# Kernel optimization log

Measured on AMD Instinct MI355X. Metric: run time of the kernel, lower is better.

## Reference

```python
import jax, jax.numpy as jnp
import numpy as np

B, S, D, H = 1, 2048, 768, 12
E, K, I = 8, 2, 1024          # routed experts, top-k, expert inter dim
IS = 2 * I                    # shared-expert inter dim (n_shared_experts * moe_inter_dim)
EPS = 1e-5
ROUTE_SCALE = 1.0


def rmsnorm(x, w, eps=EPS):
    xf = x.astype(jnp.float32)
    return (xf * jax.lax.rsqrt(jnp.mean(xf * xf, axis=-1, keepdims=True) + eps)).astype(x.dtype) * w


def setup_inputs() -> dict:
    key = jax.random.key(0)
    ks = jax.random.split(key, 8)
    sc = 0.02
    return {
        "x": jax.random.normal(ks[0], (B, S, D), jnp.float32),
        "norm1_w": jnp.ones((D,), jnp.float32),
        "norm3_w": jnp.ones((D,), jnp.float32),
        "gate_w": jax.random.normal(ks[1], (E, D), jnp.float32) * sc,
        "w1": jax.random.normal(ks[2], (E, I, D), jnp.float32) * sc,
        "b1": jnp.zeros((E, I), jnp.float32),
        "w2": jax.random.normal(ks[3], (E, D, I), jnp.float32) * sc,
        "b2": jnp.zeros((E, D), jnp.float32),
        "w3": jax.random.normal(ks[4], (E, I, D), jnp.float32) * sc,
        "b3": jnp.zeros((E, I), jnp.float32),
        "fc1_w": jax.random.normal(ks[5], (IS, D), jnp.float32) * sc,
        "fc1_b": jnp.zeros((IS,), jnp.float32),
        "fc2_w": jax.random.normal(ks[6], (D, IS), jnp.float32) * sc,
        "fc2_b": jnp.zeros((D,), jnp.float32),
    }


def _forward(x, norm1_w, norm3_w, gate_w, w1, b1, w2, b2, w3, b3,
             fc1_w, fc1_b, fc2_w, fc2_b):
    b, s, d = x.shape
    hd = d // H

    # ---- self-attention (no qkv/out projections in the original module) ----
    xn = rmsnorm(x, norm1_w)
    qkv = xn.reshape(b, s, H, hd).transpose(0, 2, 1, 3)      # [b,h,s,hd]
    scores = jnp.einsum("bhqd,bhkd->bhqk", qkv, qkv) / np.sqrt(hd)
    attn = jax.nn.softmax(scores, axis=-1)
    ao = jnp.einsum("bhqk,bhkd->bhqd", attn, qkv)
    attn_out = ao.transpose(0, 2, 1, 3).reshape(b, s, d)
    out = x + attn_out

    # ---- MoE on norm3(out) ----
    xf = rmsnorm(out, norm3_w).reshape(-1, d)                # [N, D]
    n = xf.shape[0]

    # Gate: softmax scoring, n_groups=1 (no group masking), no bias (dim != 7168)
    logits = xf @ gate_w.T                                    # [N, E]
    sc = jax.nn.softmax(logits.astype(jnp.float32), axis=-1)  # max-subtract folded in
    _, idx = jax.lax.top_k(sc, K)                             # [N, K]
    weights = jnp.take_along_axis(sc, idx, axis=-1)
    weights = jnp.clip(weights, 1e-7) * ROUTE_SCALE
    weights = weights.astype(xf.dtype)

    # combine matrix: per-token dense expert weights (zeros for unselected)
    cmb = jnp.zeros((n, E), xf.dtype).at[jnp.arange(n)[:, None], idx].add(weights)

    # SwiGLU experts, batched over E (zero combine weight == not dispatched)
    a = jnp.einsum("nd,eid->nei", xf, w1) + b1                # [N,E,I]
    g = jnp.einsum("nd,eid->nei", xf, w3) + b3
    h = jax.nn.silu(a) * g
    eo = jnp.einsum("nei,edi->ned", h, w2) + b2               # [N,E,D]
    y = jnp.einsum("ned,ne->nd", eo, cmb)

    # shared experts (SiLU MLP)
    z = jax.nn.silu(xf @ fc1_w.T + fc1_b) @ fc2_w.T + fc2_b

    moe_out = (y + z).reshape(b, s, d)
    return out + moe_out


def reference(x, norm1_w, norm3_w, gate_w, w1, b1, w2, b2, w3, b3,
              fc1_w, fc1_b, fc2_w, fc2_b):
    return _forward(x, norm1_w, norm3_w, gate_w, w1, b1, w2, b2, w3, b3,
                    fc1_w, fc1_b, fc2_w, fc2_b)
```

## Files before the change

kernel.cpp:

```cpp
#include <hip/hip_runtime.h>
#include <math.h>

#define SEQ    2048
#define DMODEL 768
#define NHEAD  12
#define NEXP   8
#define IDIM   1024
#define ISH    2048
#define KVS    4
#define NE2    10

typedef unsigned short u16;
typedef short s16x8 __attribute__((ext_vector_type(8)));
typedef u16   u16x8 __attribute__((ext_vector_type(8)));
typedef float f32x4 __attribute__((ext_vector_type(4)));

#define MFMA_BF16(a, b, c) __builtin_amdgcn_mfma_f32_16x16x32_bf16((a), (b), (c), 0, 0, 0)

__device__ __forceinline__ void glds16(const void* g, void* l) {
  __builtin_amdgcn_global_load_lds(
      (const __attribute__((address_space(1))) unsigned int*)g,
      (__attribute__((address_space(3))) unsigned int*)l, 16, 0, 0);
}

__device__ __forceinline__ u16 f2b(float f) {
  unsigned int u = __float_as_uint(f);
  unsigned int r = u + 0x7fffu + ((u >> 16) & 1u);
  return (u16)(r >> 16);
}
__device__ __forceinline__ float b2f(u16 v) {
  return __uint_as_float(((unsigned int)v) << 16);
}

__global__ __launch_bounds__(256) void cvt_all_kernel(
    const float* __restrict__ w1, const float* __restrict__ w3, const float* __restrict__ w2,
    const float* __restrict__ fc1, const float* __restrict__ fc2,
    u16* __restrict__ w1b, u16* __restrict__ w3b, u16* __restrict__ w2b,
    u16* __restrict__ fc1b, u16* __restrict__ fc2b, int* __restrict__ counts) {
  if (blockIdx.x == 0 && threadIdx.x < 16) counts[threadIdx.x] = 0;
  long i = (long)blockIdx.x * 256 + threadIdx.x;
  const long NW8 = (long)NEXP * IDIM * DMODEL / 8;
  const long NF8 = (long)ISH * DMODEL / 8;
  const float* s; u16* d; long o;
  if      (i < NW8)             { s = w1;  d = w1b;  o = i; }
  else if (i < 2 * NW8)         { s = w3;  d = w3b;  o = i - NW8; }
  else if (i < 3 * NW8)         { s = w2;  d = w2b;  o = i - 2 * NW8; }
  else if (i < 3 * NW8 + NF8)   { s = fc1; d = fc1b; o = i - 3 * NW8; }
  else if (i < 3 * NW8 + 2*NF8) { s = fc2; d = fc2b; o = i - 3 * NW8 - NF8; }
  else return;
  float4 a = ((const float4*)s)[2 * o], b = ((const float4*)s)[2 * o + 1];
  u16x8 v;
  v[0] = f2b(a.x); v[1] = f2b(a.y); v[2] = f2b(a.z); v[3] = f2b(a.w);
  v[4] = f2b(b.x); v[5] = f2b(b.y); v[6] = f2b(b.z); v[7] = f2b(b.w);
  ((u16x8*)d)[o] = v;
}

__global__ __launch_bounds__(256) void rmsnorm_kernel(const float* __restrict__ in,
                                                      const float* __restrict__ w,
                                                      u16* __restrict__ outb) {
  int row = blockIdx.x;
  int tid = threadIdx.x;
  const float* r = in + (size_t)row * DMODEL;
  float v0 = r[tid], v1 = r[tid + 256], v2 = r[tid + 512];
  float ss = v0 * v0 + v1 * v1 + v2 * v2;
  __shared__ float red[256];
  red[tid] = ss;
  __syncthreads();
  for (int s = 128; s > 0; s >>= 1) {
    if (tid < s) red[tid] += red[tid + s];
    __syncthreads();
  }
  float rms = rsqrtf(red[0] * (1.f / DMODEL) + 1e-5f);
  u16* ob = outb + (size_t)row * DMODEL;
  ob[tid]       = f2b(v0 * rms * w[tid]);
  ob[tid + 256] = f2b(v1 * rms * w[tid + 256]);
  ob[tid + 512] = f2b(v2 * rms * w[tid + 512]);
}

__global__ __launch_bounds__(256) void attn_kernel(const u16* __restrict__ xnb,
                                                   u16* __restrict__ Opart,
                                                   float* __restrict__ Mpart,
                                                   float* __restrict__ Lpart) {
  __shared__ u16 Qs[64][72];
  __shared__ u16 Ks[64][72];
  __shared__ u16 Vt[64][72];
  __shared__ u16 Ps[64][72];
  const int h = blockIdx.y, kvs = blockIdx.z;
  const int q0 = blockIdx.x * 64;
  const int tid = threadIdx.x;
  const int lane = tid & 63, w = tid >> 6;
  const int quad = lane >> 4, l15 = lane & 15;
  const size_t hoff = (size_t)h * 64;

  for (int cc = tid; cc < 512; cc += 256) {
    int row = cc >> 3, col8 = (cc & 7) * 8;
    *(u16x8*)&Qs[row][col8] = *(const u16x8*)(xnb + (size_t)(q0 + row) * DMODEL + hoff + col8);
  }
  __syncthreads();
  const s16x8 aq0 = *(const s16x8*)&Qs[16 * w + l15][quad * 8];
  const s16x8 aq1 = *(const s16x8*)&Qs[16 * w + l15][32 + quad * 8];

  f32x4 o[4] = {};
  float mrow[4], lrow[4];
#pragma unroll
  for (int r = 0; r < 4; r++) { mrow[r] = -INFINITY; lrow[r] = 0.f; }

  const int it0 = kvs * (SEQ / 64 / KVS);
  for (int it = 0; it < SEQ / 64 / KVS; it++) {
    const int k0 = (it0 + it) * 64;
    for (int cc = tid; cc < 512; cc += 256) {
      int row = cc >> 3, col8 = (cc & 7) * 8;
      *(u16x8*)&Ks[row][col8] = *(const u16x8*)(xnb + (size_t)(k0 + row) * DMODEL + hoff + col8);
    }
    __syncthreads();

    {
      const int rp = tid & 31, dc = ((tid >> 5) & 7) * 8;
      u16x8 v0 = *(const u16x8*)&Ks[2 * rp][dc];
      u16x8 v1 = *(const u16x8*)&Ks[2 * rp + 1][dc];
#pragma unroll
      for (int j = 0; j < 8; j++) {
        *(unsigned int*)&Vt[dc + j][2 * rp] =
            (unsigned int)v0[j] | ((unsigned int)v1[j] << 16);
      }
    }

    f32x4 s4[4] = {};
#pragma unroll
    for (int jt = 0; jt < 4; jt++) {
      s16x8 b0 = *(const s16x8*)&Ks[16 * jt + l15][quad * 8];
      s16x8 b1 = *(const s16x8*)&Ks[16 * jt + l15][32 + quad * 8];
      s4[jt] = MFMA_BF16(aq0, b0, s4[jt]);
      s4[jt] = MFMA_BF16(aq1, b1, s4[jt]);
      s4[jt] *= 0.125f;
    }

#pragma unroll
    for (int r = 0; r < 4; r++) {
      float mx = mrow[r];
#pragma unroll
      for (int jt = 0; jt < 4; jt++) mx = fmaxf(mx, s4[jt][r]);
#pragma unroll
      for (int m = 1; m <= 8; m <<= 1) mx = fmaxf(mx, __shfl_xor(mx, m, 64));
      float al = __expf(mrow[r] - mx);
      mrow[r] = mx;
      float pv[4], sum = 0.f;
#pragma unroll
      for (int jt = 0; jt < 4; jt++) { pv[jt] = __expf(s4[jt][r] - mx); sum += pv[jt]; }
#pragma unroll
      for (int m = 1; m <= 8; m <<= 1) sum += __shfl_xor(sum, m, 64);
      lrow[r] = lrow[r] * al + sum;
#pragma unroll
      for (int jt = 0; jt < 4; jt++) o[jt][r] *= al;
#pragma unroll
      for (int jt = 0; jt < 4; jt++) Ps[16 * w + quad * 4 + r][16 * jt + l15] = f2b(pv[jt]);
    }
    __syncthreads();

    s16x8 ap0 = *(const s16x8*)&Ps[16 * w + l15][quad * 8];
    s16x8 ap1 = *(const s16x8*)&Ps[16 * w + l15][32 + quad * 8];
#pragma unroll
    for (int jt = 0; jt < 4; jt++) {
      s16x8 bv0 = *(const s16x8*)&Vt[16 * jt + l15][quad * 8];
      s16x8 bv1 = *(const s16x8*)&Vt[16 * jt + l15][32 + quad * 8];
      o[jt] = MFMA_BF16(ap0, bv0, o[jt]);
      o[jt] = MFMA_BF16(ap1, bv1, o[jt]);
    }
  }

  const size_t base = ((size_t)kvs * NHEAD + h) * SEQ;
#pragma unroll
  for (int r = 0; r < 4; r++) {
    int q = q0 + 16 * w + quad * 4 + r;
#pragma unroll
    for (int jt = 0; jt < 4; jt++)
      Opart[(base + q) * 64 + 16 * jt + l15] = f2b(o[jt][r]);
    if (l15 == 0) {
      Mpart[base + q] = mrow[r];
      Lpart[base + q] = lrow[r];
    }
  }
}

__global__ __launch_bounds__(256) void fused_post_kernel(
    const u16* __restrict__ Opart, const float* __restrict__ Mpart,
    const float* __restrict__ Lpart, const float* __restrict__ x,
    const float* __restrict__ n3w, const float* __restrict__ gw,
    u16* __restrict__ xfb, float* __restrict__ out,
    int* __restrict__ counts, int* __restrict__ toklist, float* __restrict__ wtlist) {
  const int t = blockIdx.x;
  const int tid = threadIdx.x;
  __shared__ float Ms[KVS * NHEAD], Ls[KVS * NHEAD];
  __shared__ float red[256];
  __shared__ float gred[4][NEXP];
  if (tid < KVS * NHEAD) {
    Ms[tid] = Mpart[(size_t)tid * SEQ + t];
    Ls[tid] = Lpart[(size_t)tid * SEQ + t];
  }
  __syncthreads();

  float val[3];
  float ss = 0.f;
#pragma unroll
  for (int ii = 0; ii < 3; ii++) {
    int c = tid + ii * 256;
    int h = c >> 6, d = c & 63;
    float M = -INFINITY;
#pragma unroll
    for (int k = 0; k < KVS; k++) M = fmaxf(M, Ms[k * NHEAD + h]);
    float L = 0.f, O = 0.f;
#pragma unroll
    for (int k = 0; k < KVS; k++) {
      float wgt = __expf(Ms[k * NHEAD + h] - M);
      L += wgt * Ls[k * NHEAD + h];
      O += wgt * b2f(Opart[((size_t)(k * NHEAD + h) * SEQ + t) * 64 + d]);
    }
    float v = x[(size_t)t * DMODEL + c] + O / L;
    out[(size_t)t * DMODEL + c] = v;
    val[ii] = v;
    ss += v * v;
  }
  red[tid] = ss;
  __syncthreads();
  for (int s = 128; s > 0; s >>= 1) {
    if (tid < s) red[tid] += red[tid + s];
    __syncthreads();
  }
  float rms = rsqrtf(red[0] * (1.f / DMODEL) + 1e-5f);

  float ge[NEXP] = {};
#pragma unroll
  for (int ii = 0; ii < 3; ii++) {
    int c = tid + ii * 256;
    float xn = val[ii] * rms * n3w[c];
    xfb[(size_t)t * DMODEL + c] = f2b(xn);
#pragma unroll
    for (int e = 0; e < NEXP; e++) ge[e] = fmaf(xn, gw[e * DMODEL + c], ge[e]);
  }
  const int lane = tid & 63, w = tid >> 6;
#pragma unroll
  for (int off = 32; off >= 1; off >>= 1)
#pragma unroll
    for (int e = 0; e < NEXP; e++) ge[e] += __shfl_xor(ge[e], off, 64);
  if (lane == 0)
#pragma unroll
    for (int e = 0; e < NEXP; e++) gred[w][e] = ge[e];
  __syncthreads();
  if (tid == 0) {
    float p[NEXP], mx = -INFINITY, s = 0.f;
#pragma unroll
    for (int e = 0; e < NEXP; e++) {
      p[e] = gred[0][e] + gred[1][e] + gred[2][e] + gred[3][e];
      mx = fmaxf(mx, p[e]);
    }
#pragma unroll
    for (int e = 0; e < NEXP; e++) { p[e] = __expf(p[e] - mx); s += p[e]; }
    int e0 = 0; float b0 = p[0];
    for (int e = 1; e < NEXP; e++) if (p[e] > b0) { b0 = p[e]; e0 = e; }
    int e1 = -1; float b1v = -1.f;
    for (int e = 0; e < NEXP; e++) if (e != e0 && p[e] > b1v) { b1v = p[e]; e1 = e; }
    float inv = 1.f / s;
    int pos0 = atomicAdd(&counts[e0], 1);
    toklist[e0 * SEQ + pos0] = t;
    wtlist[e0 * SEQ + pos0] = fmaxf(b0 * inv, 1e-7f);
    int pos1 = atomicAdd(&counts[e1], 1);
    toklist[e1 * SEQ + pos1] = t;
    wtlist[e1 * SEQ + pos1] = fmaxf(b1v * inv, 1e-7f);
  }
}

__global__ __launch_bounds__(256) void gemm1_kernel(
    const u16* __restrict__ xfb,
    const u16* __restrict__ w1b, const u16* __restrict__ w3b, const u16* __restrict__ fc1b,
    const float* __restrict__ b1, const float* __restrict__ b3, const float* __restrict__ fc1_b,
    const int* __restrict__ counts, const int* __restrict__ toklist, u16* __restrict__ hb) {
  __shared__ u16 As[64][32];
  __shared__ u16 W1s[128][32];
  __shared__ u16 W3s[128][32];
  __shared__ int rIdx[64];
  const int e = blockIdx.z;
  const bool routed = (e < NEXP);
  int cnt, off;
  if (routed) {
    cnt = counts[e];
    off = 0;
    for (int i = 0; i < e; i++) off += counts[i];
  } else {
    cnt = SEQ;
    off = 2 * SEQ + (e - NEXP) * SEQ;
  }
  const int m0 = blockIdx.y * 64;
  if (m0 >= cnt) return;
  const int n0 = blockIdx.x * 128;
  const int tid = threadIdx.x;
  if (tid < 64) {
    int rr = m0 + tid;
    rIdx[tid] = routed ? toklist[e * SEQ + (rr < cnt ? rr : cnt - 1)] : rr;
  }
  __syncthreads();
  const u16* W1 = routed ? w1b + (size_t)e * IDIM * DMODEL
                         : fc1b + (size_t)(e - NEXP) * IDIM * DMODEL;
  const u16* W3 = w3b + (size_t)(routed ? e : 0) * IDIM * DMODEL;

  const int lane = tid & 63, w = tid >> 6;
  const int quad = lane >> 4, l15 = lane & 15;
  const int wy = w >> 1, wx = w & 1;
  const int rsub = lane >> 2, c8 = (lane & 3) * 8;
  const u16* Ap   = xfb + (size_t)rIdx[16 * w + rsub] * DMODEL + c8;
  const u16* W1p0 = W1 + (size_t)(n0 + 32 * w + rsub) * DMODEL + c8;
  const u16* W1p1 = W1 + (size_t)(n0 + 32 * w + 16 + rsub) * DMODEL + c8;
  const u16* W3p0 = W3 + (size_t)(n0 + 32 * w + rsub) * DMODEL + c8;
  const u16* W3p1 = W3 + (size_t)(n0 + 32 * w + 16 + rsub) * DMODEL + c8;

  f32x4 acc1[2][4] = {};
  f32x4 acc3[2][4] = {};
  for (int k0 = 0; k0 < DMODEL; k0 += 32) {
    glds16(Ap + k0, &As[16 * w][0]);
    glds16(W1p0 + k0, &W1s[32 * w][0]);
    glds16(W1p1 + k0, &W1s[32 * w + 16][0]);
    if (routed) {
      glds16(W3p0 + k0, &W3s[32 * w][0]);
      glds16(W3p1 + k0, &W3s[32 * w + 16][0]);
    }
    __syncthreads();
    s16x8 af[2], w1f[4];
#pragma unroll
    for (int i = 0; i < 2; i++) af[i] = *(const s16x8*)&As[32 * wy + 16 * i + l15][quad * 8];
#pragma unroll
    for (int j = 0; j < 4; j++) w1f[j] = *(const s16x8*)&W1s[64 * wx + 16 * j + l15][quad * 8];
#pragma unroll
    for (int i = 0; i < 2; i++)
#pragma unroll
      for (int j = 0; j < 4; j++)
        acc1[i][j] = MFMA_BF16(af[i], w1f[j], acc1[i][j]);
    if (routed) {
      s16x8 w3f[4];
#pragma unroll
      for (int j = 0; j < 4; j++) w3f[j] = *(const s16x8*)&W3s[64 * wx + 16 * j + l15][quad * 8];
#pragma unroll
      for (int i = 0; i < 2; i++)
#pragma unroll
        for (int j = 0; j < 4; j++)
          acc3[i][j] = MFMA_BF16(af[i], w3f[j], acc3[i][j]);
    }
    __syncthreads();
  }

#pragma unroll
  for (int j = 0; j < 4; j++) {
    int n = n0 + 64 * wx + 16 * j + l15;
    float b1v = routed ? b1[e * IDIM + n] : fc1_b[(e - NEXP) * IDIM + n];
    float b3v = routed ? b3[e * IDIM + n] : 0.f;
#pragma unroll
    for (int i = 0; i < 2; i++) {
#pragma unroll
      for (int r = 0; r < 4; r++) {
        int rr = m0 + 32 * wy + 16 * i + quad * 4 + r;
        if (rr < cnt) {
          float a = acc1[i][j][r] + b1v;
          float g = routed ? (acc3[i][j][r] + b3v) : 1.f;
          float hv = a / (1.f + __expf(-a)) * g;
          hb[(size_t)(off + rr) * IDIM + n] = f2b(hv);
        }
      }
    }
  }
}

__global__ __launch_bounds__(256) void gemm2_kernel(
    const u16* __restrict__ hb,
    const u16* __restrict__ w2b, const u16* __restrict__ fc2b,
    const float* __restrict__ b2, const float* __restrict__ fc2_b,
    const int* __restrict__ counts, const int* __restrict__ toklist,
    const float* __restrict__ wtlist, float* __restrict__ out) {
  __shared__ u16 As[64][32];
  __shared__ u16 Ws[128][32];
  const int e = blockIdx.z;
  const bool routed = (e < NEXP);
  int cnt, off;
  if (routed) {
    cnt = counts[e];
    off = 0;
    for (int i = 0; i < e; i++) off += counts[i];
  } else {
    cnt = SEQ;
    off = 2 * SEQ + (e - NEXP) * SEQ;
  }
  const int m0 = blockIdx.y * 64;
  if (m0 >= cnt) return;
  const int n0 = blockIdx.x * 128;
  const int tid = threadIdx.x;

  const u16* Wb; int ldw, kof;
  if (routed) { Wb = w2b + (size_t)e * DMODEL * IDIM; ldw = IDIM; kof = 0; }
  else        { Wb = fc2b;                            ldw = ISH;  kof = (e - NEXP) * IDIM; }

  const int lane = tid & 63, w = tid >> 6;
  const int quad = lane >> 4, l15 = lane & 15;
  const int wy = w >> 1, wx = w & 1;
  const int rsub = lane >> 2, c8 = (lane & 3) * 8;
  int ra = m0 + 16 * w + rsub; ra = off + (ra < cnt ? ra : cnt - 1);
  const u16* Ap  = hb + (size_t)ra * IDIM + c8;
  const u16* Wp0 = Wb + (size_t)(n0 + 32 * w + rsub) * ldw + kof + c8;
  const u16* Wp1 = Wb + (size_t)(n0 + 32 * w + 16 + rsub) * ldw + kof + c8;

  f32x4 acc[2][4] = {};
  for (int k0 = 0; k0 < IDIM; k0 += 32) {
    glds16(Ap + k0, &As[16 * w][0]);
    glds16(Wp0 + k0, &Ws[32 * w][0]);
    glds16(Wp1 + k0, &Ws[32 * w + 16][0]);
    __syncthreads();
    s16x8 af[2], wf[4];
#pragma unroll
    for (int i = 0; i < 2; i++) af[i] = *(const s16x8*)&As[32 * wy + 16 * i + l15][quad * 8];
#pragma unroll
    for (int j = 0; j < 4; j++) wf[j] = *(const s16x8*)&Ws[64 * wx + 16 * j + l15][quad * 8];
#pragma unroll
    for (int i = 0; i < 2; i++)
#pragma unroll
      for (int j = 0; j < 4; j++)
        acc[i][j] = MFMA_BF16(af[i], wf[j], acc[i][j]);
    __syncthreads();
  }

#pragma unroll
  for (int j = 0; j < 4; j++) {
    int n = n0 + 64 * wx + 16 * j + l15;
    float bv = routed ? b2[e * DMODEL + n] : (e == NEXP ? fc2_b[n] : 0.f);
#pragma unroll
    for (int i = 0; i < 2; i++) {
#pragma unroll
      for (int r = 0; r < 4; r++) {
        int rr = m0 + 32 * wy + 16 * i + quad * 4 + r;
        if (rr < cnt) {
          int tok; float wt;
          if (routed) { tok = toklist[e * SEQ + rr]; wt = wtlist[e * SEQ + rr]; }
          else        { tok = rr;                    wt = 1.f; }
          atomicAdd(&out[(size_t)tok * DMODEL + n], wt * (acc[i][j][r] + bv));
        }
      }
    }
  }
}

extern "C" void kernel_launch(void* const* d_in, const int* in_sizes, int n_in,
                              void* d_out, int out_size, void* d_ws, size_t ws_size,
                              hipStream_t stream) {
  const float* x       = (const float*)d_in[0];
  const float* norm1_w = (const float*)d_in[1];
  const float* norm3_w = (const float*)d_in[2];
  const float* gate_w  = (const float*)d_in[3];
  const float* w1      = (const float*)d_in[4];
  const float* b1      = (const float*)d_in[5];
  const float* w2      = (const float*)d_in[6];
  const float* b2      = (const float*)d_in[7];
  const float* w3      = (const float*)d_in[8];
  const float* b3      = (const float*)d_in[9];
  const float* fc1_w   = (const float*)d_in[10];
  const float* fc1_b   = (const float*)d_in[11];
  const float* fc2_w   = (const float*)d_in[12];
  const float* fc2_b   = (const float*)d_in[13];
  float* out = (float*)d_out;

  char* p = (char*)d_ws;
  u16*   xnb    = (u16*)p;   p += (size_t)SEQ * DMODEL * 2;
  u16*   xfb    = (u16*)p;   p += (size_t)SEQ * DMODEL * 2;
  u16*   hb     = (u16*)p;   p += (size_t)4 * SEQ * IDIM * 2;
  u16*   Opart  = (u16*)p;   p += (size_t)KVS * NHEAD * SEQ * 64 * 2;
  float* Mpart  = (float*)p; p += (size_t)KVS * NHEAD * SEQ * 4;
  float* Lpart  = (float*)p; p += (size_t)KVS * NHEAD * SEQ * 4;
  u16*   w1b    = (u16*)p;   p += (size_t)NEXP * IDIM * DMODEL * 2;
  u16*   w3b    = (u16*)p;   p += (size_t)NEXP * IDIM * DMODEL * 2;
  u16*   w2b    = (u16*)p;   p += (size_t)NEXP * DMODEL * IDIM * 2;
  u16*   fc1b   = (u16*)p;   p += (size_t)ISH * DMODEL * 2;
  u16*   fc2b   = (u16*)p;   p += (size_t)DMODEL * ISH * 2;
  int*   counts = (int*)p;   p += 256;
  int*   toklist= (int*)p;   p += (size_t)NEXP * SEQ * 4;
  float* wtlist = (float*)p; p += (size_t)NEXP * SEQ * 4;

  const long NW8 = (long)NEXP * IDIM * DMODEL / 8;
  const long NF8 = (long)ISH * DMODEL / 8;
  const int cvt_blocks = (int)((3 * NW8 + 2 * NF8 + 255) / 256);
  cvt_all_kernel<<<cvt_blocks, 256, 0, stream>>>(w1, w3, w2, fc1_w, fc2_w,
                                                 w1b, w3b, w2b, fc1b, fc2b, counts);
  rmsnorm_kernel<<<SEQ, 256, 0, stream>>>(x, norm1_w, xnb);
  attn_kernel<<<dim3(SEQ / 64, NHEAD, KVS), 256, 0, stream>>>(xnb, Opart, Mpart, Lpart);
  fused_post_kernel<<<SEQ, 256, 0, stream>>>(Opart, Mpart, Lpart, x, norm3_w, gate_w,
                                             xfb, out, counts, toklist, wtlist);
  gemm1_kernel<<<dim3(IDIM / 128, SEQ / 64, NE2), 256, 0, stream>>>(
      xfb, w1b, w3b, fc1b, b1, b3, fc1_b, counts, toklist, hb);
  gemm2_kernel<<<dim3(DMODEL / 128, SEQ / 64, NE2), 256, 0, stream>>>(
      hb, w2b, fc2b, b2, fc2_b, counts, toklist, wtlist, out);
  (void)in_sizes; (void)n_in; (void)out_size; (void)ws_size;
}
```

Baseline: 352.8 us.

## Merge weight conversion with rmsnorm, widen GEMM K-step, remap blocks per XCD

Folds the bf16 weight conversion and the first rmsnorm into one launch to save a kernel launch. Both MoE GEMMs now stage 64-wide K chunks per barrier instead of 32, halving the number of syncs and doubling MFMAs between them. The 3D grids are flattened into a 1D grid whose block index is remapped so that consecutive tiles of the same expert land on the same XCD (groups of 8), aiming at better L2 reuse of expert weights. The cost is more shared memory and registers per block, which may reduce occupancy.

```diff
diff --git a/kernel.cpp b/kernel.cpp
--- a/kernel.cpp
+++ b/kernel.cpp
@@ -32,38 +32,38 @@
   return __uint_as_float(((unsigned int)v) << 16);
 }
 
-__global__ __launch_bounds__(256) void cvt_all_kernel(
+#define CVT_BLOCKS 10752
+
+__global__ __launch_bounds__(256) void prep_kernel(
     const float* __restrict__ w1, const float* __restrict__ w3, const float* __restrict__ w2,
     const float* __restrict__ fc1, const float* __restrict__ fc2,
     u16* __restrict__ w1b, u16* __restrict__ w3b, u16* __restrict__ w2b,
-    u16* __restrict__ fc1b, u16* __restrict__ fc2b, int* __restrict__ counts) {
-  if (blockIdx.x == 0 && threadIdx.x < 16) counts[threadIdx.x] = 0;
-  long i = (long)blockIdx.x * 256 + threadIdx.x;
-  const long NW8 = (long)NEXP * IDIM * DMODEL / 8;
-  const long NF8 = (long)ISH * DMODEL / 8;
-  const float* s; u16* d; long o;
-  if      (i < NW8)             { s = w1;  d = w1b;  o = i; }
-  else if (i < 2 * NW8)         { s = w3;  d = w3b;  o = i - NW8; }
-  else if (i < 3 * NW8)         { s = w2;  d = w2b;  o = i - 2 * NW8; }
-  else if (i < 3 * NW8 + NF8)   { s = fc1; d = fc1b; o = i - 3 * NW8; }
-  else if (i < 3 * NW8 + 2*NF8) { s = fc2; d = fc2b; o = i - 3 * NW8 - NF8; }
-  else return;
-  float4 a = ((const float4*)s)[2 * o], b = ((const float4*)s)[2 * o + 1];
-  u16x8 v;
-  v[0] = f2b(a.x); v[1] = f2b(a.y); v[2] = f2b(a.z); v[3] = f2b(a.w);
-  v[4] = f2b(b.x); v[5] = f2b(b.y); v[6] = f2b(b.z); v[7] = f2b(b.w);
-  ((u16x8*)d)[o] = v;
-}
-
-__global__ __launch_bounds__(256) void rmsnorm_kernel(const float* __restrict__ in,
-                                                      const float* __restrict__ w,
-                                                      u16* __restrict__ outb) {
-  int row = blockIdx.x;
-  int tid = threadIdx.x;
-  const float* r = in + (size_t)row * DMODEL;
+    u16* __restrict__ fc1b, u16* __restrict__ fc2b, int* __restrict__ counts,
+    const float* __restrict__ x, const float* __restrict__ norm1_w, u16* __restrict__ xnb) {
+  __shared__ float red[256];
+  const int tid = threadIdx.x;
+  if (blockIdx.x < CVT_BLOCKS) {
+    if (blockIdx.x == 0 && tid < 16) counts[tid] = 0;
+    long i = (long)blockIdx.x * 256 + tid;
+    const long NW8 = (long)NEXP * IDIM * DMODEL / 8;
+    const long NF8 = (long)ISH * DMODEL / 8;
+    const float* s; u16* d; long o;
+    if      (i < NW8)             { s = w1;  d = w1b;  o = i; }
+    else if (i < 2 * NW8)         { s = w3;  d = w3b;  o = i - NW8; }
+    else if (i < 3 * NW8)         { s = w2;  d = w2b;  o = i - 2 * NW8; }
+    else if (i < 3 * NW8 + NF8)   { s = fc1; d = fc1b; o = i - 3 * NW8; }
+    else                          { s = fc2; d = fc2b; o = i - 3 * NW8 - NF8; }
+    float4 a = ((const float4*)s)[2 * o], b = ((const float4*)s)[2 * o + 1];
+    u16x8 v;
+    v[0] = f2b(a.x); v[1] = f2b(a.y); v[2] = f2b(a.z); v[3] = f2b(a.w);
+    v[4] = f2b(b.x); v[5] = f2b(b.y); v[6] = f2b(b.z); v[7] = f2b(b.w);
+    ((u16x8*)d)[o] = v;
+    return;
+  }
+  const int row = blockIdx.x - CVT_BLOCKS;
+  const float* r = x + (size_t)row * DMODEL;
   float v0 = r[tid], v1 = r[tid + 256], v2 = r[tid + 512];
   float ss = v0 * v0 + v1 * v1 + v2 * v2;
-  __shared__ float red[256];
   red[tid] = ss;
   __syncthreads();
   for (int s = 128; s > 0; s >>= 1) {
@@ -71,10 +71,10 @@
     __syncthreads();
   }
   float rms = rsqrtf(red[0] * (1.f / DMODEL) + 1e-5f);
-  u16* ob = outb + (size_t)row * DMODEL;
-  ob[tid]       = f2b(v0 * rms * w[tid]);
-  ob[tid + 256] = f2b(v1 * rms * w[tid + 256]);
-  ob[tid + 512] = f2b(v2 * rms * w[tid + 512]);
+  u16* ob = xnb + (size_t)row * DMODEL;
+  ob[tid]       = f2b(v0 * rms * norm1_w[tid]);
+  ob[tid + 256] = f2b(v1 * rms * norm1_w[tid + 256]);
+  ob[tid + 512] = f2b(v2 * rms * norm1_w[tid + 512]);
 }
 
 __global__ __launch_bounds__(256) void attn_kernel(const u16* __restrict__ xnb,
@@ -274,11 +274,16 @@
     const u16* __restrict__ w1b, const u16* __restrict__ w3b, const u16* __restrict__ fc1b,
     const float* __restrict__ b1, const float* __restrict__ b3, const float* __restrict__ fc1_b,
     const int* __restrict__ counts, const int* __restrict__ toklist, u16* __restrict__ hb) {
-  __shared__ u16 As[64][32];
-  __shared__ u16 W1s[128][32];
-  __shared__ u16 W3s[128][32];
+  __shared__ u16 As0[64][32],  As1[64][32];
+  __shared__ u16 W1s0[128][32], W1s1[128][32];
+  __shared__ u16 W3s0[128][32], W3s1[128][32];
   __shared__ int rIdx[64];
-  const int e = blockIdx.z;
+  const int L = blockIdx.x;
+  const int g = L & 7, s = L >> 3;
+  const int T = g * 320 + s;
+  const int e = T >> 8;
+  const int rem = T & 255;
+  const int mt = rem >> 3, nt = rem & 7;
   const bool routed = (e < NEXP);
   int cnt, off;
   if (routed) {
@@ -289,9 +294,9 @@
     cnt = SEQ;
     off = 2 * SEQ + (e - NEXP) * SEQ;
   }
-  const int m0 = blockIdx.y * 64;
+  const int m0 = mt * 64;
   if (m0 >= cnt) return;
-  const int n0 = blockIdx.x * 128;
+  const int n0 = nt * 128;
   const int tid = threadIdx.x;
   if (tid < 64) {
     int rr = m0 + tid;
@@ -314,34 +319,52 @@
 
   f32x4 acc1[2][4] = {};
   f32x4 acc3[2][4] = {};
-  for (int k0 = 0; k0 < DMODEL; k0 += 32) {
-    glds16(Ap + k0, &As[16 * w][0]);
-    glds16(W1p0 + k0, &W1s[32 * w][0]);
-    glds16(W1p1 + k0, &W1s[32 * w + 16][0]);
+  for (int k0 = 0; k0 < DMODEL; k0 += 64) {
+    glds16(Ap + k0,        &As0[16 * w][0]);
+    glds16(Ap + k0 + 32,   &As1[16 * w][0]);
+    glds16(W1p0 + k0,      &W1s0[32 * w][0]);
+    glds16(W1p1 + k0,      &W1s0[32 * w + 16][0]);
+    glds16(W1p0 + k0 + 32, &W1s1[32 * w][0]);
+    glds16(W1p1 + k0 + 32, &W1s1[32 * w + 16][0]);
     if (routed) {
-      glds16(W3p0 + k0, &W3s[32 * w][0]);
-      glds16(W3p1 + k0, &W3s[32 * w + 16][0]);
-    }
-    __syncthreads();
-    s16x8 af[2], w1f[4];
-#pragma unroll
-    for (int i = 0; i < 2; i++) af[i] = *(const s16x8*)&As[32 * wy + 16 * i + l15][quad * 8];
-#pragma unroll
-    for (int j = 0; j < 4; j++) w1f[j] = *(const s16x8*)&W1s[64 * wx + 16 * j + l15][quad * 8];
+      glds16(W3p0 + k0,      &W3s0[32 * w][0]);
+      glds16(W3p1 + k0,      &W3s0[32 * w + 16][0]);
+      glds16(W3p0 + k0 + 32, &W3s1[32 * w][0]);
+      glds16(W3p1 + k0 + 32, &W3s1[32 * w + 16][0]);
+    }
+    __syncthreads();
+    s16x8 af0[2], af1[2], w1f0[4], w1f1[4];
+#pragma unroll
+    for (int i = 0; i < 2; i++) {
+      af0[i] = *(const s16x8*)&As0[32 * wy + 16 * i + l15][quad * 8];
+      af1[i] = *(const s16x8*)&As1[32 * wy + 16 * i + l15][quad * 8];
+    }
+#pragma unroll
+    for (int j = 0; j < 4; j++) {
+      w1f0[j] = *(const s16x8*)&W1s0[64 * wx + 16 * j + l15][quad * 8];
+      w1f1[j] = *(const s16x8*)&W1s1[64 * wx + 16 * j + l15][quad * 8];
+    }
 #pragma unroll
     for (int i = 0; i < 2; i++)
 #pragma unroll
-      for (int j = 0; j < 4; j++)
-        acc1[i][j] = MFMA_BF16(af[i], w1f[j], acc1[i][j]);
+      for (int j = 0; j < 4; j++) {
+        acc1[i][j] = MFMA_BF16(af0[i], w1f0[j], acc1[i][j]);
+        acc1[i][j] = MFMA_BF16(af1[i], w1f1[j], acc1[i][j]);
+      }
     if (routed) {
-      s16x8 w3f[4];
-#pragma unroll
-      for (int j = 0; j < 4; j++) w3f[j] = *(const s16x8*)&W3s[64 * wx + 16 * j + l15][quad * 8];
+      s16x8 w3f0[4], w3f1[4];
+#pragma unroll
+      for (int j = 0; j < 4; j++) {
+        w3f0[j] = *(const s16x8*)&W3s0[64 * wx + 16 * j + l15][quad * 8];
+        w3f1[j] = *(const s16x8*)&W3s1[64 * wx + 16 * j + l15][quad * 8];
+      }
 #pragma unroll
       for (int i = 0; i < 2; i++)
 #pragma unroll
-        for (int j = 0; j < 4; j++)
-          acc3[i][j] = MFMA_BF16(af[i], w3f[j], acc3[i][j]);
+        for (int j = 0; j < 4; j++) {
+          acc3[i][j] = MFMA_BF16(af0[i], w3f0[j], acc3[i][j]);
+          acc3[i][j] = MFMA_BF16(af1[i], w3f1[j], acc3[i][j]);
+        }
     }
     __syncthreads();
   }
@@ -358,8 +381,8 @@
         int rr = m0 + 32 * wy + 16 * i + quad * 4 + r;
         if (rr < cnt) {
           float a = acc1[i][j][r] + b1v;
-          float g = routed ? (acc3[i][j][r] + b3v) : 1.f;
-          float hv = a / (1.f + __expf(-a)) * g;
+          float gg = routed ? (acc3[i][j][r] + b3v) : 1.f;
+          float hv = a / (1.f + __expf(-a)) * gg;
           hb[(size_t)(off + rr) * IDIM + n] = f2b(hv);
         }
       }
@@ -373,9 +396,14 @@
     const float* __restrict__ b2, const float* __restrict__ fc2_b,
     const int* __restrict__ counts, const int* __restrict__ toklist,
     const float* __restrict__ wtlist, float* __restrict__ out) {
-  __shared__ u16 As[64][32];
-  __shared__ u16 Ws[128][32];
-  const int e = blockIdx.z;
+  __shared__ u16 As0[64][32],  As1[64][32];
+  __shared__ u16 Ws0[128][32], Ws1[128][32];
+  const int L = blockIdx.x;
+  const int g = L & 7, s = L >> 3;
+  const int T = g * 240 + s;
+  const int e = T / 192;
+  const int rem = T - e * 192;
+  const int mt = rem / 6, nt = rem - mt * 6;
   const bool routed = (e < NEXP);
   int cnt, off;
   if (routed) {
@@ -386,9 +414,9 @@
     cnt = SEQ;
     off = 2 * SEQ + (e - NEXP) * SEQ;
   }
-  const int m0 = blockIdx.y * 64;
+  const int m0 = mt * 64;
   if (m0 >= cnt) return;
-  const int n0 = blockIdx.x * 128;
+  const int n0 = nt * 128;
   const int tid = threadIdx.x;
 
   const u16* Wb; int ldw, kof;
@@ -405,21 +433,32 @@
   const u16* Wp1 = Wb + (size_t)(n0 + 32 * w + 16 + rsub) * ldw + kof + c8;
 
   f32x4 acc[2][4] = {};
-  for (int k0 = 0; k0 < IDIM; k0 += 32) {
-    glds16(Ap + k0, &As[16 * w][0]);
-    glds16(Wp0 + k0, &Ws[32 * w][0]);
-    glds16(Wp1 + k0, &Ws[32 * w + 16][0]);
-    __syncthreads();
-    s16x8 af[2], wf[4];
-#pragma unroll
-    for (int i = 0; i < 2; i++) af[i] = *(const s16x8*)&As[32 * wy + 16 * i + l15][quad * 8];
-#pragma unroll
-    for (int j = 0; j < 4; j++) wf[j] = *(const s16x8*)&Ws[64 * wx + 16 * j + l15][quad * 8];
+  for (int k0 = 0; k0 < IDIM; k0 += 64) {
+    glds16(Ap + k0,        &As0[16 * w][0]);
+    glds16(Ap + k0 + 32,   &As1[16 * w][0]);
+    glds16(Wp0 + k0,       &Ws0[32 * w][0]);
+    glds16(Wp1 + k0,       &Ws0[32 * w + 16][0]);
+    glds16(Wp0 + k0 + 32,  &Ws1[32 * w][0]);
+    glds16(Wp1 + k0 + 32,  &Ws1[32 * w + 16][0]);
+    __syncthreads();
+    s16x8 af0[2], af1[2], wf0[4], wf1[4];
+#pragma unroll
+    for (int i = 0; i < 2; i++) {
+      af0[i] = *(const s16x8*)&As0[32 * wy + 16 * i + l15][quad * 8];
+      af1[i] = *(const s16x8*)&As1[32 * wy + 16 * i + l15][quad * 8];
+    }
+#pragma unroll
+    for (int j = 0; j < 4; j++) {
+      wf0[j] = *(const s16x8*)&Ws0[64 * wx + 16 * j + l15][quad * 8];
+      wf1[j] = *(const s16x8*)&Ws1[64 * wx + 16 * j + l15][quad * 8];
+    }
 #pragma unroll
     for (int i = 0; i < 2; i++)
 #pragma unroll
-      for (int j = 0; j < 4; j++)
-        acc[i][j] = MFMA_BF16(af[i], wf[j], acc[i][j]);
+      for (int j = 0; j < 4; j++) {
+        acc[i][j] = MFMA_BF16(af0[i], wf0[j], acc[i][j]);
+        acc[i][j] = MFMA_BF16(af1[i], wf1[j], acc[i][j]);
+      }
     __syncthreads();
   }
 
@@ -478,18 +517,14 @@
   int*   toklist= (int*)p;   p += (size_t)NEXP * SEQ * 4;
   float* wtlist = (float*)p; p += (size_t)NEXP * SEQ * 4;
 
-  const long NW8 = (long)NEXP * IDIM * DMODEL / 8;
-  const long NF8 = (long)ISH * DMODEL / 8;
-  const int cvt_blocks = (int)((3 * NW8 + 2 * NF8 + 255) / 256);
-  cvt_all_kernel<<<cvt_blocks, 256, 0, stream>>>(w1, w3, w2, fc1_w, fc2_w,
-                                                 w1b, w3b, w2b, fc1b, fc2b, counts);
-  rmsnorm_kernel<<<SEQ, 256, 0, stream>>>(x, norm1_w, xnb);
+  prep_kernel<<<CVT_BLOCKS + SEQ, 256, 0, stream>>>(
+      w1, w3, w2, fc1_w, fc2_w, w1b, w3b, w2b, fc1b, fc2b, counts, x, norm1_w, xnb);
   attn_kernel<<<dim3(SEQ / 64, NHEAD, KVS), 256, 0, stream>>>(xnb, Opart, Mpart, Lpart);
   fused_post_kernel<<<SEQ, 256, 0, stream>>>(Opart, Mpart, Lpart, x, norm3_w, gate_w,
                                              xfb, out, counts, toklist, wtlist);
-  gemm1_kernel<<<dim3(IDIM / 128, SEQ / 64, NE2), 256, 0, stream>>>(
+  gemm1_kernel<<<2560, 256, 0, stream>>>(
       xfb, w1b, w3b, fc1b, b1, b3, fc1_b, counts, toklist, hb);
-  gemm2_kernel<<<dim3(DMODEL / 128, SEQ / 64, NE2), 256, 0, stream>>>(
+  gemm2_kernel<<<1920, 256, 0, stream>>>(
       hb, w2b, fc2b, b2, fc2_b, counts, toklist, wtlist, out);
   (void)in_sizes; (void)n_in; (void)out_size; (void)ws_size;
 }
```

Result: slower. 376.4 us (+6.7%).
